# Optimization experiments

Hardware: AMD Instinct MI355X
Metric: run time of the kernel (lower is better)

The kernel has to match this reference:

```python
import jax, jax.numpy as jnp
import numpy as np

NUM_HEADS = 16
NEG_BIG = -1.0e9


def setup_inputs() -> dict:
    key = jax.random.key(0)
    k1, k2, k3 = jax.random.split(key, 3)
    B, S, D = 2, 2048, 1024
    x = jax.random.normal(k1, (B, S, D), dtype=jnp.float32)
    qkv_weights = jax.random.normal(k2, (D, 3 * D), dtype=jnp.float32) * (1.0 / np.sqrt(D))
    output_weights = jax.random.normal(k3, (D, D), dtype=jnp.float32) * (1.0 / np.sqrt(D))
    return {"x": x, "qkv_weights": qkv_weights, "output_weights": output_weights}


def reference(x, qkv_weights, output_weights):
    B, S, D = x.shape
    H = NUM_HEADS
    hd = D // H
    qkv = jnp.einsum('bsd,de->bse', x, qkv_weights)  # [B,S,3D]
    q, k, v = jnp.split(qkv, 3, axis=-1)
    # [B,H,S,hd]
    q = q.reshape(B, S, H, hd).transpose(0, 2, 1, 3)
    k = k.reshape(B, S, H, hd).transpose(0, 2, 1, 3)
    v = v.reshape(B, S, H, hd).transpose(0, 2, 1, 3)
    scores = jnp.einsum('bhqd,bhkd->bhqk', q, k)  # unscaled, matches original masked path
    # original bug: when masked, softmax is applied to UNSCALED scores with mask
    tril = jnp.tril(jnp.ones((S, S), dtype=scores.dtype))
    masked = scores * tril + NEG_BIG * (1.0 - tril)
    attn = jax.nn.softmax(masked, axis=-1)
    heads = jnp.einsum('bhqk,bhkd->bhqd', attn, v)  # [B,H,S,hd]
    merged = heads.transpose(0, 2, 1, 3).reshape(B, S, D)
    return jnp.einsum('bsd,de->bse', merged, output_weights)
```

## Files before the change

kernel.cpp:

```cpp
#include <hip/hip_runtime.h>
#include <stdint.h>

using u16 = unsigned short;
typedef __attribute__((ext_vector_type(8))) _Float16 half8;
typedef __attribute__((ext_vector_type(4))) float f32x4;
typedef __attribute__((ext_vector_type(4))) unsigned short u16x4;

#define S_LEN 2048
#define D_MODEL 1024
#define NHEAD 16
#define HDIM 64

__device__ __forceinline__ u16 f2h_bits(float f){
    _Float16 h = (_Float16)f;
    return __builtin_bit_cast(u16, h);
}
__device__ __forceinline__ float h2f_bits(u16 v){
    return (float)__builtin_bit_cast(_Float16, v);
}

typedef __attribute__((address_space(1))) void gvoid;
typedef __attribute__((address_space(3))) void lvoid;
__device__ __forceinline__ void gload_lds16(const u16* g, u16* l){
    __builtin_amdgcn_global_load_lds((gvoid*)(uintptr_t)g, (lvoid*)l, 16, 0, 0);
}

__global__ __launch_bounds__(256) void k_cvt_x(const float* __restrict__ x, u16* __restrict__ xh){
    int i = blockIdx.x*256 + threadIdx.x;
    float4 v = reinterpret_cast<const float4*>(x)[i];
    u16x4 o;
    o.x = f2h_bits(v.x); o.y = f2h_bits(v.y); o.z = f2h_bits(v.z); o.w = f2h_bits(v.w);
    reinterpret_cast<u16x4*>(xh)[i] = o;
}

__global__ __launch_bounds__(256) void k_cvt_w(const float* __restrict__ W0, u16* __restrict__ T0,
                                               const float* __restrict__ W1, u16* __restrict__ T1){
    __shared__ float tt[32][33];
    int bx = blockIdx.x;
    const float* W; u16* WT; int N, n0;
    if (bx < 96){ W = W0; WT = T0; N = 3072; n0 = bx*32; }
    else        { W = W1; WT = T1; N = 1024; n0 = (bx-96)*32; }
    int k0 = blockIdx.y*32;
    int tx = threadIdx.x & 31, ty = threadIdx.x >> 5;
    #pragma unroll
    for (int i=0;i<4;++i) tt[ty+8*i][tx] = W[(size_t)(k0+ty+8*i)*N + n0+tx];
    __syncthreads();
    #pragma unroll
    for (int i=0;i<4;++i) WT[(size_t)(n0+ty+8*i)*1024 + k0+tx] = f2h_bits(tt[tx][ty+8*i]);
}

template<int EPI>
__global__ __launch_bounds__(256) void k_gemm(const u16* __restrict__ A, const u16* __restrict__ BT,
                                              float* __restrict__ Cf, u16* __restrict__ Qh,
                                              u16* __restrict__ Kh, u16* __restrict__ Vt){
    constexpr int Kd = 1024;
    __shared__ u16 As[2*128*32];
    __shared__ u16 Bs[2*128*32];
    int nwg = gridDim.x;
    int cpx = nwg >> 3;
    int wg  = ((int)blockIdx.x & 7)*cpx + ((int)blockIdx.x >> 3);
    int tm = wg & 31, tn = wg >> 5;
    int t = threadIdx.x;
    int w = t >> 6, lane = t & 63;
    int lr = lane & 15, lg = lane >> 4;
    int wm = (w>>1)*64, wn = (w&1)*64;
    int m0 = tm*128 + wm, n0 = tn*128 + wn;

    const u16* aG = A  + (size_t)(tm*128 + (t>>2))*Kd + (t&3)*8;
    const u16* bG = BT + (size_t)(tn*128 + (t>>2))*Kd + (t&3)*8;
    u16* aL = As + (t>>2)*32 + (t&3)*8;
    u16* bL = Bs + (t>>2)*32 + (t&3)*8;

    auto stage = [&](int buf, int kk){
        gload_lds16(aG + kk, aL + buf*4096);
        gload_lds16(aG + kk + (size_t)64*Kd, aL + buf*4096 + 64*32);
        gload_lds16(bG + kk, bL + buf*4096);
        gload_lds16(bG + kk + (size_t)64*Kd, bL + buf*4096 + 64*32);
    };

    f32x4 acc[4][4];
    #pragma unroll
    for (int i=0;i<4;++i)
        #pragma unroll
        for (int j=0;j<4;++j) acc[i][j] = (f32x4){0.f,0.f,0.f,0.f};

    stage(0, 0);
    __syncthreads();
    for (int kk=0; kk<Kd; kk+=32){
        int cur = (kk>>5) & 1;
        if (kk+32 < Kd) stage(cur^1, kk+32);

        half8 av[4], bv[4];
        #pragma unroll
        for (int mf=0;mf<4;++mf) av[mf] = *reinterpret_cast<const half8*>(&As[cur*4096 + (wm+mf*16+lr)*32 + lg*8]);
        #pragma unroll
        for (int nf=0;nf<4;++nf) bv[nf] = *reinterpret_cast<const half8*>(&Bs[cur*4096 + (wn+nf*16+lr)*32 + lg*8]);
        __builtin_amdgcn_s_setprio(1);
        #pragma unroll
        for (int mf=0;mf<4;++mf)
            #pragma unroll
            for (int nf=0;nf<4;++nf)
                acc[mf][nf] = __builtin_amdgcn_mfma_f32_16x16x32_f16(av[mf], bv[nf], acc[mf][nf], 0,0,0);
        __builtin_amdgcn_s_setprio(0);
        __syncthreads();
    }

    if (EPI == 0){
        #pragma unroll
        for (int mf=0;mf<4;++mf)
            #pragma unroll
            for (int nf=0;nf<4;++nf)
                #pragma unroll
                for (int j=0;j<4;++j)
                    Cf[(size_t)(m0+mf*16+lg*4+j)*D_MODEL + n0+nf*16+lr] = acc[mf][nf][j];
    } else {
        #pragma unroll
        for (int mf=0;mf<4;++mf){
            int r0 = m0 + mf*16 + lg*4;
            int b  = r0 >> 11, s = r0 & 2047;
            #pragma unroll
            for (int nf=0;nf<4;++nf){
                int col = n0 + nf*16 + lr;
                int which = col >> 10;
                int d  = col & 1023;
                int h  = d >> 6, di = d & 63;
                int bh = b*NHEAD + h;
                if (which == 2){
                    u16x4 pv;
                    pv.x = f2h_bits(acc[mf][nf][0]);
                    pv.y = f2h_bits(acc[mf][nf][1]);
                    pv.z = f2h_bits(acc[mf][nf][2]);
                    pv.w = f2h_bits(acc[mf][nf][3]);
                    *reinterpret_cast<u16x4*>(Vt + ((size_t)bh*HDIM + di)*S_LEN + s) = pv;
                } else {
                    u16* dst = (which==0 ? Qh : Kh) + ((size_t)bh*S_LEN + s)*HDIM + di;
                    #pragma unroll
                    for (int j=0;j<4;++j) dst[(size_t)j*HDIM] = f2h_bits(acc[mf][nf][j]);
                }
            }
        }
    }
}

__global__ __launch_bounds__(256,3) void k_attn(const u16* __restrict__ Q, const u16* __restrict__ K,
                                                const u16* __restrict__ Vt, u16* __restrict__ Mg,
                                                u16* __restrict__ On, float* __restrict__ Ml,
                                                float* __restrict__ Ll){
    __shared__ u16 Kl[2*64*64];
    __shared__ u16 Vl[2*64*64];
    __shared__ u16 plds[4][32][72];
    int t = threadIdx.x;
    int w = t >> 6, lane = t & 63;
    int lr = lane & 15, lg = lane >> 4;
    int blk = blockIdx.x;
    int bh  = blk & 31;
    int p   = blk >> 5;
    int qb, ktLo, ktHi, part; bool split;
    if (p < 8)      { qb = p;    ktLo = 0;      ktHi = 2*p+2;   split = false; part = 0; }
    else if (p < 16){ qb = 23-p; ktLo = 0;      ktHi = qb+1;    split = true;  part = 0; }
    else            { qb = 31-p; ktLo = qb+1;   ktHi = 2*qb+2;  split = true;  part = 1; }
    int q0w = qb*128 + w*32;
    int b = bh >> 4, h = bh & 15;
    int pid = split ? ((bh<<3) + (qb-8))*2 + part : 0;
    const u16* Qp = Q  + (size_t)bh*S_LEN*HDIM;
    const u16* Kp = K  + (size_t)bh*S_LEN*HDIM;
    const u16* Vp = Vt + (size_t)bh*HDIM*S_LEN;

    int c0 = t, c1 = t + 256;
    int r0 = c0 >> 3, s0 = 8*((c0 & 7) ^ (r0 & 7));
    int r1 = c1 >> 3, s1 = 8*((c1 & 7) ^ (r1 & 7));
    const u16* Ks0 = Kp + (size_t)r0*HDIM + s0;
    const u16* Ks1 = Kp + (size_t)r1*HDIM + s1;
    const u16* Vs0 = Vp + (size_t)r0*S_LEN + s0;
    const u16* Vs1 = Vp + (size_t)r1*S_LEN + s1;
    u16* Kd0 = Kl + c0*8; u16* Kd1 = Kl + c1*8;
    u16* Vd0 = Vl + c0*8; u16* Vd1 = Vl + c1*8;

    auto stageKV = [&](int buf, int kt){
        int kbase = kt*64;
        gload_lds16(Ks0 + (size_t)kbase*HDIM, Kd0 + buf*4096);
        gload_lds16(Ks1 + (size_t)kbase*HDIM, Kd1 + buf*4096);
        gload_lds16(Vs0 + kbase, Vd0 + buf*4096);
        gload_lds16(Vs1 + kbase, Vd1 + buf*4096);
    };

    half8 qf[2][2];
    #pragma unroll
    for (int qi=0;qi<2;++qi)
        #pragma unroll
        for (int ks=0;ks<2;++ks){
            half8 v = *reinterpret_cast<const half8*>(Qp + (size_t)(q0w+qi*16+lr)*HDIM + ks*32 + lg*8);
            #pragma unroll
            for (int j=0;j<8;++j) v[j] = v[j] * (_Float16)1.44269504f;
            qf[qi][ks] = v;
        }

    f32x4 oacc[2][4];
    float mrow[2], lrow[2];
    #pragma unroll
    for (int mf=0;mf<2;++mf){
        #pragma unroll
        for (int nf=0;nf<4;++nf) oacc[mf][nf] = (f32x4){0.f,0.f,0.f,0.f};
        mrow[mf] = -1e30f; lrow[mf] = 0.f;
    }

    int lastkt = (q0w + 31) >> 6;
    int swz = (lr & 7)*8;
    int nT = ktHi - ktLo;

    stageKV(0, ktLo);
    __syncthreads();
    for (int i=0; i<nT; ++i){
        int kt = ktLo + i;
        int cur = i & 1;
        if (i+1 < nT) stageKV(cur^1, kt+1);

        if (kt <= lastkt){
            const u16* Kb = Kl + cur*4096;
            const u16* Vb = Vl + cur*4096;
            int kbase = kt*64;
            half8 kfr[4][2];
            #pragma unroll
            for (int kf=0;kf<4;++kf)
                #pragma unroll
                for (int ks=0;ks<2;++ks)
                    kfr[kf][ks] = *reinterpret_cast<const half8*>(Kb + (kf*16+lr)*64 + ((ks*32 + lg*8) ^ swz));
            f32x4 sc[4][2];
            #pragma unroll
            for (int kf=0;kf<4;++kf)
                #pragma unroll
                for (int qi=0;qi<2;++qi) sc[kf][qi] = (f32x4){0.f,0.f,0.f,0.f};
            __builtin_amdgcn_s_setprio(1);
            #pragma unroll
            for (int kf=0;kf<4;++kf)
                #pragma unroll
                for (int qi=0;qi<2;++qi)
                    #pragma unroll
                    for (int ks=0;ks<2;++ks)
                        sc[kf][qi] = __builtin_amdgcn_mfma_f32_16x16x32_f16(kfr[kf][ks], qf[qi][ks], sc[kf][qi], 0,0,0);
            __builtin_amdgcn_s_setprio(0);

            half8 vf[4][2];
            #pragma unroll
            for (int nf=0;nf<4;++nf)
                #pragma unroll
                for (int kh=0;kh<2;++kh)
                    vf[nf][kh] = *reinterpret_cast<const half8*>(Vb + (nf*16+lr)*64 + ((kh*32 + lg*8) ^ swz));

            if (kt == lastkt){
                #pragma unroll
                for (int kf=0;kf<4;++kf)
                    #pragma unroll
                    for (int qi=0;qi<2;++qi)
                        #pragma unroll
                        for (int j=0;j<4;++j)
                            if (kbase+kf*16+lg*4+j > q0w+qi*16+lr) sc[kf][qi][j] = -1e9f;
            }

            float pmax[2];
            #pragma unroll
            for (int qi=0;qi<2;++qi){
                float t0 = fmaxf(fmaxf(sc[0][qi][0], sc[0][qi][1]), fmaxf(sc[0][qi][2], sc[0][qi][3]));
                float t1 = fmaxf(fmaxf(sc[1][qi][0], sc[1][qi][1]), fmaxf(sc[1][qi][2], sc[1][qi][3]));
                float t2 = fmaxf(fmaxf(sc[2][qi][0], sc[2][qi][1]), fmaxf(sc[2][qi][2], sc[2][qi][3]));
                float t3 = fmaxf(fmaxf(sc[3][qi][0], sc[3][qi][1]), fmaxf(sc[3][qi][2], sc[3][qi][3]));
                float tm = fmaxf(fmaxf(t0,t1), fmaxf(t2,t3));
                tm = fmaxf(tm, __shfl_xor(tm,16));
                tm = fmaxf(tm, __shfl_xor(tm,32));
                pmax[qi] = tm;
            }
            bool need = (pmax[0] > mrow[0]+8.0f) || (pmax[1] > mrow[1]+8.0f);
            if (__any(need)){
                float aq[2];
                #pragma unroll
                for (int qi=0;qi<2;++qi){
                    float mnew = fmaxf(mrow[qi], pmax[qi]);
                    aq[qi] = __builtin_amdgcn_exp2f(mrow[qi] - mnew);
                    mrow[qi] = mnew;
                    lrow[qi] *= aq[qi];
                }
                float am[2][4];
                #pragma unroll
                for (int mf=0;mf<2;++mf)
                    #pragma unroll
                    for (int j=0;j<4;++j) am[mf][j] = __shfl(aq[mf], lg*4+j);
                #pragma unroll
                for (int mf=0;mf<2;++mf)
                    #pragma unroll
                    for (int nf=0;nf<4;++nf)
                        #pragma unroll
                        for (int j=0;j<4;++j) oacc[mf][nf][j] *= am[mf][j];
            }
            #pragma unroll
            for (int qi=0;qi<2;++qi){
                float m = mrow[qi];
                float rs = 0.f;
                #pragma unroll
                for (int kf=0;kf<4;++kf)
                    #pragma unroll
                    for (int j=0;j<4;++j){
                        float e = __builtin_amdgcn_exp2f(sc[kf][qi][j] - m);
                        sc[kf][qi][j] = e;
                        rs += e;
                    }
                rs += __shfl_xor(rs,16);
                rs += __shfl_xor(rs,32);
                lrow[qi] += rs;
            }
            #pragma unroll
            for (int kf=0;kf<4;++kf)
                #pragma unroll
                for (int qi=0;qi<2;++qi){
                    u16x4 pk;
                    pk.x = f2h_bits(sc[kf][qi][0]);
                    pk.y = f2h_bits(sc[kf][qi][1]);
                    pk.z = f2h_bits(sc[kf][qi][2]);
                    pk.w = f2h_bits(sc[kf][qi][3]);
                    *reinterpret_cast<u16x4*>(&plds[w][qi*16+lr][kf*16+lg*4]) = pk;
                }
            half8 pa[2][2];
            #pragma unroll
            for (int mf=0;mf<2;++mf)
                #pragma unroll
                for (int kh=0;kh<2;++kh)
                    pa[mf][kh] = *reinterpret_cast<const half8*>(&plds[w][mf*16+lr][kh*32 + lg*8]);
            __builtin_amdgcn_s_setprio(1);
            #pragma unroll
            for (int mf=0;mf<2;++mf)
                #pragma unroll
                for (int nf=0;nf<4;++nf)
                    #pragma unroll
                    for (int kh=0;kh<2;++kh)
                        oacc[mf][nf] = __builtin_amdgcn_mfma_f32_16x16x32_f16(pa[mf][kh], vf[nf][kh], oacc[mf][nf], 0,0,0);
            __builtin_amdgcn_s_setprio(0);
        }
        __syncthreads();
    }

    float linv[2][4];
    #pragma unroll
    for (int mf=0;mf<2;++mf)
        #pragma unroll
        for (int j=0;j<4;++j) linv[mf][j] = 1.0f/__shfl(lrow[mf], lg*4+j);
    if (!split){
        #pragma unroll
        for (int mf=0;mf<2;++mf)
            #pragma unroll
            for (int nf=0;nf<4;++nf)
                #pragma unroll
                for (int j=0;j<4;++j)
                    Mg[(size_t)(b*S_LEN + q0w + mf*16 + lg*4 + j)*D_MODEL + h*HDIM + nf*16 + lr]
                        = f2h_bits(oacc[mf][nf][j]*linv[mf][j]);
    } else {
        #pragma unroll
        for (int mf=0;mf<2;++mf)
            #pragma unroll
            for (int nf=0;nf<4;++nf)
                #pragma unroll
                for (int j=0;j<4;++j)
                    On[pid*8192 + (w*32 + mf*16 + lg*4 + j)*64 + nf*16 + lr]
                        = f2h_bits(oacc[mf][nf][j]*linv[mf][j]);
        if (lg == 0){
            #pragma unroll
            for (int qi=0;qi<2;++qi){
                Ml[pid*128 + w*32 + qi*16 + lr] = mrow[qi];
                Ll[pid*128 + w*32 + qi*16 + lr] = lrow[qi];
            }
        }
    }
}

__global__ __launch_bounds__(256) void k_comb(const u16* __restrict__ On, const float* __restrict__ Ml,
                                              const float* __restrict__ Ll, u16* __restrict__ Mg){
    int blk = blockIdx.x;
    int bh = blk & 31;
    int q8 = (blk >> 5) & 7;
    int rq = blk >> 8;
    int qb = 8 + q8;
    int b = bh >> 4, h = bh & 15;
    int t = threadIdx.x;
    int r  = rq*16 + (t >> 4);
    int cc = (t & 15) * 4;
    int pid0 = ((bh<<3) + q8)*2, pid1 = pid0 + 1;
    float m1 = Ml[pid0*128 + r], m2 = Ml[pid1*128 + r];
    float l1 = Ll[pid0*128 + r], l2 = Ll[pid1*128 + r];
    float M  = fmaxf(m1, m2);
    float w1 = l1*__builtin_amdgcn_exp2f(m1 - M);
    float w2 = l2*__builtin_amdgcn_exp2f(m2 - M);
    float inv = 1.0f/(w1 + w2);
    u16x4 o1 = *reinterpret_cast<const u16x4*>(On + (size_t)pid0*8192 + r*64 + cc);
    u16x4 o2 = *reinterpret_cast<const u16x4*>(On + (size_t)pid1*8192 + r*64 + cc);
    u16x4 o;
    #pragma unroll
    for (int j=0;j<4;++j)
        o[j] = f2h_bits((w1*h2f_bits(o1[j]) + w2*h2f_bits(o2[j]))*inv);
    *reinterpret_cast<u16x4*>(Mg + (size_t)(b*S_LEN + qb*128 + r)*D_MODEL + h*HDIM + cc) = o;
}

extern "C" void kernel_launch(void* const* d_in, const int* in_sizes, int n_in,
                              void* d_out, int out_size, void* d_ws, size_t ws_size,
                              hipStream_t stream) {
    const float* x    = (const float*)d_in[0];
    const float* wqkv = (const float*)d_in[1];
    const float* wout = (const float*)d_in[2];
    float* out = (float*)d_out;
    char* ws = (char*)d_ws;

    const size_t MB = 1u<<20;
    u16* xh     = (u16*)(ws + 0*MB);
    u16* wqkvT  = (u16*)(ws + 8*MB);
    u16* woutT  = (u16*)(ws + 14*MB);
    u16* Qh     = (u16*)(ws + 16*MB);
    u16* Kh     = (u16*)(ws + 24*MB);
    u16* Vt     = (u16*)(ws + 32*MB);
    u16* Mg     = (u16*)(ws + 40*MB);
    u16* On     = (u16*)(ws + 48*MB);
    float* Ml   = (float*)(ws + 56*MB);
    float* Ll   = (float*)(ws + 56*MB + 256*1024);

    k_cvt_x <<<4096, 256, 0, stream>>>(x, xh);
    k_cvt_w <<<dim3(128,32), 256, 0, stream>>>(wqkv, wqkvT, wout, woutT);
    k_gemm<1><<<768, 256, 0, stream>>>(xh, wqkvT, nullptr, Qh, Kh, Vt);
    k_attn  <<<768, 256, 0, stream>>>(Qh, Kh, Vt, Mg, On, Ml, Ll);
    k_comb  <<<2048, 256, 0, stream>>>(On, Ml, Ll, Mg);
    k_gemm<0><<<256, 256, 0, stream>>>(Mg, woutT, out, nullptr, nullptr, nullptr);
}
```

Before: 115.9 us.

## Rebalance causal attention work with table-driven multi-way KV splits

Replaces the fixed scheme, where only the larger query blocks split their key range in two, with constant lookup tables. The tables split query blocks 4-15 into two to four key-range partitions and pack whole blocks 0-3 into the same grid, growing it from 768 to 1280 workgroups. The combine kernel now merges a variable number of partial outputs per row using log-sum-exp weights. The goal is more even per-workgroup work and better CU occupancy, at the cost of more partial-output traffic and a larger combine pass.

```diff
diff --git a/kernel.cpp b/kernel.cpp
--- a/kernel.cpp
+++ b/kernel.cpp
@@ -24,6 +24,13 @@
 __device__ __forceinline__ void gload_lds16(const u16* g, u16* l){
     __builtin_amdgcn_global_load_lds((gvoid*)(uintptr_t)g, (lvoid*)l, 16, 0, 0);
 }
+
+__device__ __constant__ signed char QB_T[40] = {3,7,7,10,11,11,11,14,14,15,15,15,15, 6,6,9,9,10,10,12,12,13,13,13,13,14,14, 2,5,5,8,8,8,9,12,12, 4,4, 1, 0};
+__device__ __constant__ signed char LO_T[40] = {0,0,8,0,0,8,16,0,8,0,8,16,24, 0,7,0,7,8,15,0,7,0,7,14,21,16,23, 0,0,6,0,6,12,14,14,20, 0,5, 0, 0};
+__device__ __constant__ signed char HI_T[40] = {8,8,16,8,8,16,24,8,16,8,16,24,32, 7,14,7,14,15,22,7,14,7,14,21,28,23,30, 6,6,12,6,12,18,20,20,26, 5,10, 4, 2};
+__device__ __constant__ signed char PO_T[40] = {-1,6,7,14,17,18,19,28,29,32,33,34,35, 4,5,11,12,15,16,20,21,24,25,26,27,30,31, -1,2,3,8,9,10,13,22,23, 0,1, -1, -1};
+__device__ __constant__ signed char NP_T[12] = {2,2,2,2,3,3,3,3,4,4,4,4};
+__device__ __constant__ signed char OF_T[12] = {0,2,4,6,8,11,14,17,20,24,28,32};
 
 __global__ __launch_bounds__(256) void k_cvt_x(const float* __restrict__ x, u16* __restrict__ xh){
     int i = blockIdx.x*256 + threadIdx.x;
@@ -154,14 +161,15 @@
     int lr = lane & 15, lg = lane >> 4;
     int blk = blockIdx.x;
     int bh  = blk & 31;
-    int p   = blk >> 5;
-    int qb, ktLo, ktHi, part; bool split;
-    if (p < 8)      { qb = p;    ktLo = 0;      ktHi = 2*p+2;   split = false; part = 0; }
-    else if (p < 16){ qb = 23-p; ktLo = 0;      ktHi = qb+1;    split = true;  part = 0; }
-    else            { qb = 31-p; ktLo = qb+1;   ktHi = 2*qb+2;  split = true;  part = 1; }
+    int pi  = blk >> 5;
+    int qb   = QB_T[pi];
+    int ktLo = LO_T[pi];
+    int ktHi = HI_T[pi];
+    int po   = PO_T[pi];
+    bool split = (po >= 0);
     int q0w = qb*128 + w*32;
     int b = bh >> 4, h = bh & 15;
-    int pid = split ? ((bh<<3) + (qb-8))*2 + part : 0;
+    int pid = split ? bh*36 + po : 0;
     const u16* Qp = Q  + (size_t)bh*S_LEN*HDIM;
     const u16* Kp = K  + (size_t)bh*S_LEN*HDIM;
     const u16* Vp = Vt + (size_t)bh*HDIM*S_LEN;
@@ -358,7 +366,7 @@
             for (int nf=0;nf<4;++nf)
                 #pragma unroll
                 for (int j=0;j<4;++j)
-                    On[pid*8192 + (w*32 + mf*16 + lg*4 + j)*64 + nf*16 + lr]
+                    On[(size_t)pid*8192 + (w*32 + mf*16 + lg*4 + j)*64 + nf*16 + lr]
                         = f2h_bits(oacc[mf][nf][j]*linv[mf][j]);
         if (lg == 0){
             #pragma unroll
@@ -374,26 +382,45 @@
                                               const float* __restrict__ Ll, u16* __restrict__ Mg){
     int blk = blockIdx.x;
     int bh = blk & 31;
-    int q8 = (blk >> 5) & 7;
-    int rq = blk >> 8;
-    int qb = 8 + q8;
+    int rest = blk >> 5;
+    int qi = rest >> 3;
+    int rq = rest & 7;
+    int qb = 4 + qi;
+    int np = NP_T[qi];
+    int base = bh*36 + OF_T[qi];
     int b = bh >> 4, h = bh & 15;
     int t = threadIdx.x;
     int r  = rq*16 + (t >> 4);
     int cc = (t & 15) * 4;
-    int pid0 = ((bh<<3) + q8)*2, pid1 = pid0 + 1;
-    float m1 = Ml[pid0*128 + r], m2 = Ml[pid1*128 + r];
-    float l1 = Ll[pid0*128 + r], l2 = Ll[pid1*128 + r];
-    float M  = fmaxf(m1, m2);
-    float w1 = l1*__builtin_amdgcn_exp2f(m1 - M);
-    float w2 = l2*__builtin_amdgcn_exp2f(m2 - M);
-    float inv = 1.0f/(w1 + w2);
-    u16x4 o1 = *reinterpret_cast<const u16x4*>(On + (size_t)pid0*8192 + r*64 + cc);
-    u16x4 o2 = *reinterpret_cast<const u16x4*>(On + (size_t)pid1*8192 + r*64 + cc);
+    float osum0=0.f, osum1=0.f, osum2=0.f, osum3=0.f, wsum=0.f;
+    float mm[4], ll[4];
+    float M = -1e30f;
+    #pragma unroll
+    for (int p=0;p<4;++p){
+        if (p < np){
+            mm[p] = Ml[(base+p)*128 + r];
+            ll[p] = Ll[(base+p)*128 + r];
+            M = fmaxf(M, mm[p]);
+        }
+    }
+    #pragma unroll
+    for (int p=0;p<4;++p){
+        if (p < np){
+            float wgt = ll[p]*__builtin_amdgcn_exp2f(mm[p] - M);
+            u16x4 ov = *reinterpret_cast<const u16x4*>(On + (size_t)(base+p)*8192 + r*64 + cc);
+            osum0 += wgt*h2f_bits(ov[0]);
+            osum1 += wgt*h2f_bits(ov[1]);
+            osum2 += wgt*h2f_bits(ov[2]);
+            osum3 += wgt*h2f_bits(ov[3]);
+            wsum  += wgt;
+        }
+    }
+    float inv = 1.0f/wsum;
     u16x4 o;
-    #pragma unroll
-    for (int j=0;j<4;++j)
-        o[j] = f2h_bits((w1*h2f_bits(o1[j]) + w2*h2f_bits(o2[j]))*inv);
+    o[0] = f2h_bits(osum0*inv);
+    o[1] = f2h_bits(osum1*inv);
+    o[2] = f2h_bits(osum2*inv);
+    o[3] = f2h_bits(osum3*inv);
     *reinterpret_cast<u16x4*>(Mg + (size_t)(b*S_LEN + qb*128 + r)*D_MODEL + h*HDIM + cc) = o;
 }
 
@@ -415,13 +442,13 @@
     u16* Vt     = (u16*)(ws + 32*MB);
     u16* Mg     = (u16*)(ws + 40*MB);
     u16* On     = (u16*)(ws + 48*MB);
-    float* Ml   = (float*)(ws + 56*MB);
-    float* Ll   = (float*)(ws + 56*MB + 256*1024);
+    float* Ml   = (float*)(ws + 67*MB);
+    float* Ll   = (float*)(ws + 67*MB + 640*1024);
 
     k_cvt_x <<<4096, 256, 0, stream>>>(x, xh);
     k_cvt_w <<<dim3(128,32), 256, 0, stream>>>(wqkv, wqkvT, wout, woutT);
     k_gemm<1><<<768, 256, 0, stream>>>(xh, wqkvT, nullptr, Qh, Kh, Vt);
-    k_attn  <<<768, 256, 0, stream>>>(Qh, Kh, Vt, Mg, On, Ml, Ll);
-    k_comb  <<<2048, 256, 0, stream>>>(On, Ml, Ll, Mg);
+    k_attn  <<<1280, 256, 0, stream>>>(Qh, Kh, Vt, Mg, On, Ml, Ll);
+    k_comb  <<<3072, 256, 0, stream>>>(On, Ml, Ll, Mg);
     k_gemm<0><<<256, 256, 0, stream>>>(Mg, woutT, out, nullptr, nullptr, nullptr);
 }
```

After: 118.2 us. No clear change (+2.0%).
